# Kernel tuning notes

Hardware: AMD Instinct MI355X
Metric: run time of the kernel (lower is better)

Reference implementation:

```python
import jax, jax.numpy as jnp
import numpy as np

N, P, Q, H_DIM, HEADS, D = 4096, 128, 128, 256, 8, 64  # D = graph_dim // heads


def setup_inputs() -> dict:
    key = jax.random.key(0)
    ks = jax.random.split(key, 6)
    s = 0.05  # small scale to keep tanh/softmax in a sane range
    return {
        "x_prices": jax.random.normal(ks[0], (N, P), jnp.float32),
        "x_news": jax.random.normal(ks[1], (N, Q), jnp.float32),
        "W_bil": jax.random.normal(ks[2], (H_DIM, P, Q), jnp.float32) * s,
        "b_bil": jax.random.normal(ks[3], (H_DIM,), jnp.float32) * s,
        "Wt": jax.random.normal(ks[4], (HEADS, D, H_DIM), jnp.float32) * s,
        "a_vec": jax.random.normal(ks[5], (HEADS, 2 * D), jnp.float32) * s,
    }


def reference(x_prices, x_news, W_bil, b_bil, Wt, a_vec):
    # nn.Bilinear: out[n,h] = sum_pq x_prices[n,p] W[h,p,q] x_news[n,q] + b[h]
    x = jnp.einsum('np,hpq,nq->nh', x_prices, W_bil, x_news) + b_bil  # (N, hidden)

    # Per-head linear transform: fc_transform (no bias). Wt: (heads, d, hidden)
    xt = jnp.einsum('nh,kdh->knd', x, Wt)  # (heads, N, d)

    # Attention score a . [x_i, x_j] split into src/dst halves -> broadcast add
    d = Wt.shape[1]
    a_src, a_dst = a_vec[:, :d], a_vec[:, d:]
    s_src = jnp.einsum('knd,kd->kn', xt, a_src)  # (heads, N)
    s_dst = jnp.einsum('knd,kd->kn', xt, a_dst)  # (heads, N)
    scores = s_src[:, :, None] + s_dst[:, None, :]  # (heads, N, N)
    scores = jnp.where(scores >= 0, scores, 0.2 * scores)  # LeakyReLU(0.2)

    attn = jax.nn.softmax(scores, axis=-1)  # softmax over neighbors j
    out = jnp.einsum('knm,kmd->knd', attn, xt)  # (heads, N, d)

    # Concatenate head outputs on feature dim, then tanh
    out = jnp.transpose(out, (1, 0, 2)).reshape(xt.shape[1], -1)  # (N, heads*d)
    return jnp.tanh(out)
```

## Files before the change

kernel.cpp:

```cpp
#include <hip/hip_runtime.h>
#include <hip/hip_bf16.h>

typedef unsigned short ushort;
typedef unsigned int uint;
typedef unsigned long long u64;
typedef _Float16 f16;

#define NN 4096
#define PP 128
#define QQ 128
#define HD 256
#define KH 8
#define DD 64
#define KK 16384

typedef _Float16 f16x2 __attribute__((ext_vector_type(2)));
typedef _Float16 f16x4 __attribute__((ext_vector_type(4)));
typedef _Float16 f16x8 __attribute__((ext_vector_type(8)));
typedef __fp16 fp16x2 __attribute__((ext_vector_type(2)));
typedef float f32x4 __attribute__((ext_vector_type(4)));

__device__ inline void async_lds16(const void* g, void* l) {
  __builtin_amdgcn_global_load_lds(
      (const __attribute__((address_space(1))) unsigned int*)g,
      (__attribute__((address_space(3))) unsigned int*)l, 16, 0, 0);
}

__global__ __launch_bounds__(256) void k0_split2(
    const float* __restrict__ W, const float* __restrict__ Wt,
    f16* __restrict__ hiW, f16* __restrict__ loW,
    f16* __restrict__ hiT, f16* __restrict__ loT) {
  const int i = (blockIdx.x * 256 + threadIdx.x) * 4;
  const float* src;
  f16 *hi, *lo;
  int off;
  if (i < HD * PP * QQ) { src = W; hi = hiW; lo = loW; off = i; }
  else { src = Wt; hi = hiT; lo = loT; off = i - HD * PP * QQ; }
  const float4 w = *(const float4*)&src[off];
  const float wf[4] = {w.x, w.y, w.z, w.w};
  f16x4 hv, lv;
#pragma unroll
  for (int j = 0; j < 4; ++j) {
    const f16 h = (f16)wf[j];
    hv[j] = h;
    lv[j] = (f16)(wf[j] - (float)h);
  }
  *(f16x4*)&hi[off] = hv;
  *(f16x4*)&lo[off] = lv;
}

__global__ __launch_bounds__(256) void k_zero4(float* __restrict__ p) {
  const int i = (blockIdx.x * 256 + threadIdx.x) * 4;
  *(float4*)&p[i] = make_float4(0.f, 0.f, 0.f, 0.f);
}

__global__ __launch_bounds__(256, 2) void k1_bilinear(
    const float* __restrict__ xp, const float* __restrict__ xn,
    const f16* __restrict__ Whi, const f16* __restrict__ Wlo,
    float* __restrict__ xout) {
  __shared__ f16 whi[256 * 32];
  __shared__ f16 wlo[256 * 32];
  __shared__ f16 zhi[128 * 40];
  __shared__ float xpt[8][128];

  const int t = threadIdx.x;
  const int n0 = blockIdx.x * 128;
  const int kb = blockIdx.y * (KK / 16);
  const int pb = kb >> 7;

  for (int idx = t; idx < 1024; idx += 256) {
    const int p = idx & 7, n = idx >> 3;
    xpt[p][n] = xp[(size_t)(n0 + n) * PP + pb + p];
  }

  const int l = t & 63, w = t >> 6;
  const int wr = (w >> 1) * 64, wc = (w & 1) * 128;

  int aoff[4], boff[8];
#pragma unroll
  for (int i = 0; i < 4; ++i)
    aoff[i] = (wr + i * 16 + (l & 15)) * 40 + (l >> 4) * 8;
#pragma unroll
  for (int j = 0; j < 8; ++j) {
    const int hr = wc + j * 16 + (l & 15);
    boff[j] = hr * 32 + (((l >> 4) ^ ((hr ^ (hr >> 2)) & 3)) * 8);
  }

  const int shb = t >> 2, seg = t & 3;
  int gsw[4];
#pragma unroll
  for (int g = 0; g < 4; ++g) {
    const int r = shb + 64 * g;
    gsw[g] = seg ^ ((r ^ (r >> 2)) & 3);
  }

  const int zn = t >> 1, zko = (t & 1) * 16;

  f32x4 acc[4][8];
#pragma unroll
  for (int i = 0; i < 4; ++i)
#pragma unroll
    for (int j = 0; j < 8; ++j) acc[i][j] = (f32x4)0.f;

  for (int c = 0; c < 32; ++c) {
    const int kc = kb + c * 32;
    const int pl = c >> 2;
    const int q0 = (c & 3) * 32;

    __syncthreads();

#pragma unroll
    for (int g = 0; g < 4; ++g) {
      const int r = shb + 64 * g;
      async_lds16(Whi + (size_t)r * KK + kc + gsw[g] * 8, whi + r * 32 + seg * 8);
      async_lds16(Wlo + (size_t)r * KK + kc + gsw[g] * 8, wlo + r * 32 + seg * 8);
    }

    {
      const float xpv = xpt[pl][zn];
      const float* xr = xn + (size_t)(n0 + zn) * QQ + q0 + zko;
      float4 v0 = ((const float4*)xr)[0];
      float4 v1 = ((const float4*)xr)[1];
      float4 v2 = ((const float4*)xr)[2];
      float4 v3 = ((const float4*)xr)[3];
      float zz[16] = {v0.x, v0.y, v0.z, v0.w, v1.x, v1.y, v1.z, v1.w,
                      v2.x, v2.y, v2.z, v2.w, v3.x, v3.y, v3.z, v3.w};
      union { uint u[8]; uint4 q[2]; } ph;
#pragma unroll
      for (int j = 0; j < 8; ++j) {
        union { fp16x2 h; uint u; } cv;
        cv.h = __builtin_amdgcn_cvt_pkrtz(xpv * zz[2 * j], xpv * zz[2 * j + 1]);
        ph.u[j] = cv.u;
      }
      const int zo = zn * 40 + zko;
      *(uint4*)&zhi[zo] = ph.q[0];
      *(uint4*)&zhi[zo + 8] = ph.q[1];
    }

    __syncthreads();

    f16x8 Ah[4];
#pragma unroll
    for (int i = 0; i < 4; ++i) Ah[i] = *(const f16x8*)&zhi[aoff[i]];
#pragma unroll
    for (int j = 0; j < 8; ++j) {
      const f16x8 Bh = *(const f16x8*)&whi[boff[j]];
      const f16x8 Bl = *(const f16x8*)&wlo[boff[j]];
#pragma unroll
      for (int i = 0; i < 4; ++i)
        acc[i][j] = __builtin_amdgcn_mfma_f32_16x16x32_f16(Ah[i], Bh, acc[i][j], 0, 0, 0);
#pragma unroll
      for (int i = 0; i < 4; ++i)
        acc[i][j] = __builtin_amdgcn_mfma_f32_16x16x32_f16(Ah[i], Bl, acc[i][j], 0, 0, 0);
    }
  }

#pragma unroll
  for (int i = 0; i < 4; ++i)
#pragma unroll
    for (int j = 0; j < 8; ++j) {
      const int row = n0 + wr + i * 16 + (l >> 4) * 4;
      const int col = wc + j * 16 + (l & 15);
#pragma unroll
      for (int r = 0; r < 4; ++r)
        atomicAdd(&xout[(size_t)(row + r) * HD + col], acc[i][j][r]);
    }
}

__global__ __launch_bounds__(256) void k23_xt(
    const float* __restrict__ x, const float* __restrict__ bb,
    const f16* __restrict__ Wthi, const f16* __restrict__ Wtlo,
    float* __restrict__ xt) {
  __shared__ f16 ah[64 * 40];
  __shared__ f16 bh[128 * 32];
  __shared__ f16 bl[128 * 32];
  const int t = threadIdx.x;
  const int n0 = blockIdx.x * 64;
  const int c0 = blockIdx.y * 128;
  const int l = t & 63, w = t >> 6;
  const int wn = (w & 1) * 32, wcc = (w >> 1) * 64;

  int aoff[2], boff[4];
#pragma unroll
  for (int i = 0; i < 2; ++i)
    aoff[i] = (wn + i * 16 + (l & 15)) * 40 + (l >> 4) * 8;
#pragma unroll
  for (int j = 0; j < 4; ++j) {
    const int hr = wcc + j * 16 + (l & 15);
    boff[j] = hr * 32 + (((l >> 4) ^ ((hr ^ (hr >> 2)) & 3)) * 8);
  }

  f32x4 acc[2][4];
#pragma unroll
  for (int i = 0; i < 2; ++i)
#pragma unroll
    for (int j = 0; j < 4; ++j) acc[i][j] = (f32x4)0.f;

  for (int kc = 0; kc < HD; kc += 32) {
    __syncthreads();
    {
      const int row = t >> 2, sg = t & 3;
      const float* xr = &x[(size_t)(n0 + row) * HD + kc + sg * 8];
      const float4 xa = ((const float4*)xr)[0];
      const float4 xb = ((const float4*)xr)[1];
      const float4 ba = *(const float4*)&bb[kc + sg * 8];
      const float4 bv = *(const float4*)&bb[kc + sg * 8 + 4];
      f16x8 o;
      o[0] = (f16)(xa.x + ba.x); o[1] = (f16)(xa.y + ba.y);
      o[2] = (f16)(xa.z + ba.z); o[3] = (f16)(xa.w + ba.w);
      o[4] = (f16)(xb.x + bv.x); o[5] = (f16)(xb.y + bv.y);
      o[6] = (f16)(xb.z + bv.z); o[7] = (f16)(xb.w + bv.w);
      *(f16x8*)&ah[row * 40 + sg * 8] = o;
    }
#pragma unroll
    for (int g = 0; g < 2; ++g) {
      const int slot = g * 256 + t;
      const int col = slot >> 2, ps = slot & 3;
      const int ls = ps ^ ((col ^ (col >> 2)) & 3);
      *(uint4*)&bh[col * 32 + ps * 8] =
          *(const uint4*)&Wthi[(size_t)(c0 + col) * HD + kc + ls * 8];
      *(uint4*)&bl[col * 32 + ps * 8] =
          *(const uint4*)&Wtlo[(size_t)(c0 + col) * HD + kc + ls * 8];
    }
    __syncthreads();
    f16x8 Af[2];
#pragma unroll
    for (int i = 0; i < 2; ++i) Af[i] = *(const f16x8*)&ah[aoff[i]];
#pragma unroll
    for (int j = 0; j < 4; ++j) {
      const f16x8 Bh = *(const f16x8*)&bh[boff[j]];
      const f16x8 Bl = *(const f16x8*)&bl[boff[j]];
#pragma unroll
      for (int i = 0; i < 2; ++i)
        acc[i][j] = __builtin_amdgcn_mfma_f32_16x16x32_f16(Af[i], Bh, acc[i][j], 0, 0, 0);
#pragma unroll
      for (int i = 0; i < 2; ++i)
        acc[i][j] = __builtin_amdgcn_mfma_f32_16x16x32_f16(Af[i], Bl, acc[i][j], 0, 0, 0);
    }
  }
#pragma unroll
  for (int i = 0; i < 2; ++i)
#pragma unroll
    for (int j = 0; j < 4; ++j) {
      const int row = n0 + wn + i * 16 + (l >> 4) * 4;
      const int colg = c0 + wcc + j * 16 + (l & 15);
      const int k = colg >> 6, d = colg & 63;
#pragma unroll
      for (int r = 0; r < 4; ++r)
        xt[((size_t)(k * NN + row + r)) * DD + d] = acc[i][j][r];
    }
}

__global__ __launch_bounds__(256) void k3_scores(
    const float* __restrict__ xt, const float* __restrict__ av,
    float* __restrict__ ssrc, float* __restrict__ sdst) {
  const int tid = blockIdx.x * 256 + threadIdx.x;
  const int k = tid >> 12;
  const float* xr = xt + (long)tid * DD;
  const float* a = av + k * (2 * DD);
  float s1 = 0.f, s2 = 0.f;
#pragma unroll
  for (int d = 0; d < DD; d += 4) {
    const float4 xv = *(const float4*)&xr[d];
    const float4 a1 = *(const float4*)&a[d];
    const float4 a2 = *(const float4*)&a[DD + d];
    s1 += xv.x * a1.x + xv.y * a1.y + xv.z * a1.z + xv.w * a1.w;
    s2 += xv.x * a2.x + xv.y * a2.y + xv.z * a2.z + xv.w * a2.w;
  }
  ssrc[tid] = s1;
  sdst[tid] = s2;
}

__global__ __launch_bounds__(256) void k4_rank(
    const float* __restrict__ sdst, float* __restrict__ vsorted,
    int* __restrict__ perm) {
  __shared__ u64 kv[4096];
  const int k = blockIdx.y, t = threadIdx.x;
  for (int i = t; i < 4096; i += 256) {
    const uint u = __float_as_uint(sdst[k * NN + i]);
    const uint key = (u & 0x80000000u) ? ~u : (u | 0x80000000u);
    kv[i] = ((u64)key << 32) | (uint)i;
  }
  __syncthreads();
  const int m = blockIdx.x * 256 + t;
  const u64 my = kv[m];
  int cnt = 0;
#pragma unroll 16
  for (int j = 0; j < 4096; ++j) cnt += (kv[j] < my) ? 1 : 0;
  const uint key = (uint)(my >> 32);
  const uint u = (key & 0x80000000u) ? (key ^ 0x80000000u) : ~key;
  vsorted[k * NN + cnt] = __uint_as_float(u);
  perm[k * NN + cnt] = (int)(my & 0xFFFFFFFFu);
}

__global__ __launch_bounds__(64) void k4b_chunksum(
    const float* __restrict__ vs, const int* __restrict__ perm,
    const float* __restrict__ xt, float* __restrict__ Chi, float* __restrict__ Clo) {
  __shared__ float rows[64][64];
  __shared__ float eh[64], el[64];
  const int c = blockIdx.x, k = blockIdx.y, t = threadIdx.x;
  const int base = k * NN + c * 64;
  {
    const float v = vs[base + t];
    eh[t] = __expf(v);
    el[t] = __expf(0.2f * v);
  }
#pragma unroll
  for (int r = 0; r < 16; ++r) {
    const int i = r * 4 + (t >> 4);
    const int p = perm[base + i];
    *(float4*)&rows[i][(t & 15) * 4] =
        *(const float4*)&xt[((size_t)(k * NN + p)) * DD + (t & 15) * 4];
  }
  __syncthreads();
  float shi = 0.f, slo = 0.f, whs = 0.f, wls = 0.f;
#pragma unroll 8
  for (int i = 0; i < 64; ++i) {
    const float val = rows[i][t];
    shi += eh[i] * val; slo += el[i] * val;
    whs += eh[i]; wls += el[i];
  }
  const int cb = (k * 64 + c) * 65;
  Chi[cb + t] = shi;
  Clo[cb + t] = slo;
  if (t == 0) { Chi[cb + 64] = whs; Clo[cb + 64] = wls; }
}

__global__ __launch_bounds__(128) void k4c_scan(
    const float* __restrict__ Chi, const float* __restrict__ Clo,
    float* __restrict__ ChiS, float* __restrict__ CloS) {
  __shared__ float schi[64 * 65];
  __shared__ float sclo[64 * 65];
  const int k = blockIdx.x, t = threadIdx.x;
  for (int idx = t; idx < 4160; idx += 128) {
    schi[idx] = Chi[k * 4160 + idx];
    sclo[idx] = Clo[k * 4160 + idx];
  }
  __syncthreads();
  if (t >= 65) return;
  float run = 0.f;
  for (int c = 0; c < 64; ++c) {
    CloS[(k * 64 + c) * 65 + t] = run;
    run += sclo[c * 65 + t];
  }
  run = 0.f;
  for (int c = 63; c >= 0; --c) {
    run += schi[c * 65 + t];
    ChiS[(k * 64 + c) * 65 + t] = run;
  }
}

__global__ __launch_bounds__(64) void k4d_expand(
    const float* __restrict__ vs, const int* __restrict__ perm,
    const float* __restrict__ xt, const float* __restrict__ ChiS,
    const float* __restrict__ CloS, float* __restrict__ Phi,
    float* __restrict__ Plo) {
  __shared__ float rows[64][64];
  __shared__ float eh[64], el[64];
  const int c = blockIdx.x, k = blockIdx.y, t = threadIdx.x;
  const int base = k * NN + c * 64;
  const int cb = (k * 64 + c) * 65;
  {
    const float v = vs[base + t];
    eh[t] = __expf(v);
    el[t] = __expf(0.2f * v);
  }
#pragma unroll
  for (int r = 0; r < 16; ++r) {
    const int i = r * 4 + (t >> 4);
    const int p = perm[base + i];
    *(float4*)&rows[i][(t & 15) * 4] =
        *(const float4*)&xt[((size_t)(k * NN + p)) * DD + (t & 15) * 4];
  }
  __syncthreads();
  float run = CloS[cb + t];
  float wrun = CloS[cb + 64];
  for (int i = 0; i < 64; ++i) {
    const size_t rb = ((size_t)(k * 4097) + c * 64 + i) * 65;
    Plo[rb + t] = run;
    if (t == 0) Plo[rb + 64] = wrun;
    run += el[i] * rows[i][t];
    wrun += el[i];
  }
  if (c == 63) {
    const size_t rb = ((size_t)(k * 4097) + 4096) * 65;
    Plo[rb + t] = run;
    if (t == 0) Plo[rb + 64] = wrun;
  }
  run = (c < 63) ? ChiS[cb + 65 + t] : 0.f;
  wrun = (c < 63) ? ChiS[cb + 65 + 64] : 0.f;
  for (int i = 63; i >= 0; --i) {
    run += eh[i] * rows[i][t];
    wrun += eh[i];
    const size_t rb = ((size_t)(k * 4097) + c * 64 + i) * 65;
    Phi[rb + t] = run;
    if (t == 0) Phi[rb + 64] = wrun;
  }
  if (c == 63) {
    const size_t rb = ((size_t)(k * 4097) + 4096) * 65;
    Phi[rb + t] = 0.f;
    if (t == 0) Phi[rb + 64] = 0.f;
  }
}

__global__ __launch_bounds__(256) void k6_final(
    const float* __restrict__ ssrc, const float* __restrict__ vsorted,
    const float* __restrict__ Phi, const float* __restrict__ Plo,
    float* __restrict__ out) {
  __shared__ float vsh[4096];
  __shared__ int posSh[4];
  const int t = threadIdx.x;
  const int q0 = blockIdx.x * 4;
  const int k = q0 >> 12;
  for (int idx = t; idx < 1024; idx += 256)
    *(float4*)&vsh[idx * 4] = *(const float4*)&vsorted[k * NN + idx * 4];
  __syncthreads();
  if (t < 4) {
    const float thr = -ssrc[q0 + t];
    int lo = 0, hi = 4096;
    while (lo < hi) {
      const int mid = (lo + hi) >> 1;
      if (vsh[mid] < thr) lo = mid + 1; else hi = mid;
    }
    posSh[t] = lo;
  }
  __syncthreads();
  const int qi = q0 + (t >> 6);
  const int d = t & 63;
  const int n = qi & 4095;
  const float u = ssrc[qi];
  const size_t rb = ((size_t)(k * 4097) + posSh[t >> 6]) * 65;
  const float eu = __expf(u), el = __expf(0.2f * u);
  const float num = eu * Phi[rb + d] + el * Plo[rb + d];
  const float den = eu * Phi[rb + 64] + el * Plo[rb + 64];
  out[(size_t)n * (KH * DD) + k * DD + d] = tanhf(num / den);
}

extern "C" void kernel_launch(void* const* d_in, const int* in_sizes, int n_in,
                              void* d_out, int out_size, void* d_ws, size_t ws_size,
                              hipStream_t stream) {
  const float* xp = (const float*)d_in[0];
  const float* xn = (const float*)d_in[1];
  const float* W = (const float*)d_in[2];
  const float* bb = (const float*)d_in[3];
  const float* Wt = (const float*)d_in[4];
  const float* av = (const float*)d_in[5];
  float* out = (float*)d_out;

  char* ws = (char*)d_ws;
  f16* Whi    = (f16*)(ws);
  f16* Wlo    = (f16*)(ws + 8388608);
  float* Phi  = (float*)(ws);
  float* Plo  = (float*)(ws + 8522240);
  float* x    = (float*)(ws + 17044480);
  float* xt   = (float*)(ws + 21238784);
  f16* Wthi   = (f16*)(ws + 31724544);
  f16* Wtlo   = (f16*)(ws + 31986688);
  float* ssrc = (float*)(ws + 32248832);
  float* sdst = (float*)(ws + 32379904);
  float* vsort= (float*)(ws + 32510976);
  int*   perm = (int*)  (ws + 32642048);
  float* Chi  = (float*)(ws + 32773120);
  float* Clo  = (float*)(ws + 32906240);
  float* ChiS = (float*)(ws + 33039360);
  float* CloS = (float*)(ws + 33172480);

  k0_split2<<<(HD * PP * QQ + KH * DD * HD) / 1024, 256, 0, stream>>>(
      W, Wt, Whi, Wlo, Wthi, Wtlo);
  k_zero4<<<(NN * HD) / 1024, 256, 0, stream>>>(x);
  k1_bilinear<<<dim3(NN / 128, 16), 256, 0, stream>>>(xp, xn, Whi, Wlo, x);
  k23_xt<<<dim3(NN / 64, 4), 256, 0, stream>>>(x, bb, Wthi, Wtlo, xt);
  k3_scores<<<(KH * NN) / 256, 256, 0, stream>>>(xt, av, ssrc, sdst);
  k4_rank<<<dim3(16, KH), 256, 0, stream>>>(sdst, vsort, perm);
  k4b_chunksum<<<dim3(64, KH), 64, 0, stream>>>(vsort, perm, xt, Chi, Clo);
  k4c_scan<<<KH, 128, 0, stream>>>(Chi, Clo, ChiS, CloS);
  k4d_expand<<<dim3(64, KH), 64, 0, stream>>>(vsort, perm, xt, ChiS, CloS, Phi, Plo);
  k6_final<<<(KH * NN) / 4, 256, 0, stream>>>(ssrc, vsort, Phi, Plo, out);
}
```

Baseline: 290.4 us.

## Fuse zeroing and score kernels, double bilinear block to 512 threads

Zeroing of the bilinear output is folded into the weight-split kernel, and the attention score dot products are computed from MFMA accumulators inside the xt kernel through a shared-memory reduction, removing two launches and a reread of xt. The bilinear kernel now uses 512 threads covering 256 rows per block, so each W tile loaded into LDS is reused across twice as many rows, halving W traffic and the number of atomic partial-sum blocks. The larger block raises LDS use and register pressure under launch_bounds(512,2), and the hidden bilinear body must index rows consistently with the new tiling.

```diff
diff --git a/kernel.cpp b/kernel.cpp
--- a/kernel.cpp
+++ b/kernel.cpp
@@ -29,8 +29,11 @@
 __global__ __launch_bounds__(256) void k0_split2(
     const float* __restrict__ W, const float* __restrict__ Wt,
     f16* __restrict__ hiW, f16* __restrict__ loW,
-    f16* __restrict__ hiT, f16* __restrict__ loT) {
-  const int i = (blockIdx.x * 256 + threadIdx.x) * 4;
+    f16* __restrict__ hiT, f16* __restrict__ loT, float* __restrict__ xz) {
+  const int tid = blockIdx.x * 256 + threadIdx.x;
+  const int i = tid * 4;
+  if (tid < (NN * HD) / 4)
+    *(float4*)&xz[i] = make_float4(0.f, 0.f, 0.f, 0.f);
   const float* src;
   f16 *hi, *lo;
   int off;
@@ -49,32 +52,28 @@
   *(f16x4*)&lo[off] = lv;
 }
 
-__global__ __launch_bounds__(256) void k_zero4(float* __restrict__ p) {
-  const int i = (blockIdx.x * 256 + threadIdx.x) * 4;
-  *(float4*)&p[i] = make_float4(0.f, 0.f, 0.f, 0.f);
-}
-
-__global__ __launch_bounds__(256, 2) void k1_bilinear(
+__global__ __launch_bounds__(512, 2) void k1_bilinear(
     const float* __restrict__ xp, const float* __restrict__ xn,
     const f16* __restrict__ Whi, const f16* __restrict__ Wlo,
     float* __restrict__ xout) {
   __shared__ f16 whi[256 * 32];
   __shared__ f16 wlo[256 * 32];
-  __shared__ f16 zhi[128 * 40];
-  __shared__ float xpt[8][128];
+  __shared__ f16 zhi[256 * 40];
+  __shared__ float xpt[8][256];
 
   const int t = threadIdx.x;
-  const int n0 = blockIdx.x * 128;
+  const int n0 = blockIdx.x * 256;
   const int kb = blockIdx.y * (KK / 16);
   const int pb = kb >> 7;
 
-  for (int idx = t; idx < 1024; idx += 256) {
+  for (int idx = t; idx < 2048; idx += 512) {
     const int p = idx & 7, n = idx >> 3;
     xpt[p][n] = xp[(size_t)(n0 + n) * PP + pb + p];
   }
 
   const int l = t & 63, w = t >> 6;
-  const int wr = (w >> 1) * 64, wc = (w & 1) * 128;
+  const int wr = (w >> 1) * 64;
+  const int wc = (w & 1) * 128;
 
   int aoff[4], boff[8];
 #pragma unroll
@@ -87,10 +86,10 @@
   }
 
   const int shb = t >> 2, seg = t & 3;
-  int gsw[4];
-#pragma unroll
-  for (int g = 0; g < 4; ++g) {
-    const int r = shb + 64 * g;
+  int gsw[2];
+#pragma unroll
+  for (int g = 0; g < 2; ++g) {
+    const int r = shb + 128 * g;
     gsw[g] = seg ^ ((r ^ (r >> 2)) & 3);
   }
 
@@ -110,8 +109,8 @@
     __syncthreads();
 
 #pragma unroll
-    for (int g = 0; g < 4; ++g) {
-      const int r = shb + 64 * g;
+    for (int g = 0; g < 2; ++g) {
+      const int r = shb + 128 * g;
       async_lds16(Whi + (size_t)r * KK + kc + gsw[g] * 8, whi + r * 32 + seg * 8);
       async_lds16(Wlo + (size_t)r * KK + kc + gsw[g] * 8, wlo + r * 32 + seg * 8);
     }
@@ -170,10 +169,13 @@
 __global__ __launch_bounds__(256) void k23_xt(
     const float* __restrict__ x, const float* __restrict__ bb,
     const f16* __restrict__ Wthi, const f16* __restrict__ Wtlo,
-    float* __restrict__ xt) {
+    const float* __restrict__ av, float* __restrict__ xt,
+    float* __restrict__ ssrc, float* __restrict__ sdst) {
   __shared__ f16 ah[64 * 40];
   __shared__ f16 bh[128 * 32];
   __shared__ f16 bl[128 * 32];
+  __shared__ float red1[2][64][17];
+  __shared__ float red2[2][64][17];
   const int t = threadIdx.x;
   const int n0 = blockIdx.x * 64;
   const int c0 = blockIdx.y * 128;
@@ -238,6 +240,32 @@
         acc[i][j] = __builtin_amdgcn_mfma_f32_16x16x32_f16(Af[i], Bl, acc[i][j], 0, 0, 0);
     }
   }
+
+  const int hh = w >> 1;
+  const int khead = (c0 >> 6) + hh;
+  float a1v[4], a2v[4];
+#pragma unroll
+  for (int j = 0; j < 4; ++j) {
+    const int d = j * 16 + (l & 15);
+    a1v[j] = av[khead * (2 * DD) + d];
+    a2v[j] = av[khead * (2 * DD) + DD + d];
+  }
+
+#pragma unroll
+  for (int i = 0; i < 2; ++i)
+#pragma unroll
+    for (int r = 0; r < 4; ++r) {
+      const int rowl = wn + i * 16 + (l >> 4) * 4 + r;
+      float p1 = 0.f, p2 = 0.f;
+#pragma unroll
+      for (int j = 0; j < 4; ++j) {
+        p1 += acc[i][j][r] * a1v[j];
+        p2 += acc[i][j][r] * a2v[j];
+      }
+      red1[hh][rowl][l & 15] = p1;
+      red2[hh][rowl][l & 15] = p2;
+    }
+
 #pragma unroll
   for (int i = 0; i < 2; ++i)
 #pragma unroll
@@ -249,26 +277,20 @@
       for (int r = 0; r < 4; ++r)
         xt[((size_t)(k * NN + row + r)) * DD + d] = acc[i][j][r];
     }
-}
-
-__global__ __launch_bounds__(256) void k3_scores(
-    const float* __restrict__ xt, const float* __restrict__ av,
-    float* __restrict__ ssrc, float* __restrict__ sdst) {
-  const int tid = blockIdx.x * 256 + threadIdx.x;
-  const int k = tid >> 12;
-  const float* xr = xt + (long)tid * DD;
-  const float* a = av + k * (2 * DD);
-  float s1 = 0.f, s2 = 0.f;
-#pragma unroll
-  for (int d = 0; d < DD; d += 4) {
-    const float4 xv = *(const float4*)&xr[d];
-    const float4 a1 = *(const float4*)&a[d];
-    const float4 a2 = *(const float4*)&a[DD + d];
-    s1 += xv.x * a1.x + xv.y * a1.y + xv.z * a1.z + xv.w * a1.w;
-    s2 += xv.x * a2.x + xv.y * a2.y + xv.z * a2.z + xv.w * a2.w;
-  }
-  ssrc[tid] = s1;
-  sdst[tid] = s2;
+
+  __syncthreads();
+  {
+    const int hh2 = t >> 7;
+    const int which = (t >> 6) & 1;
+    const int row = t & 63;
+    const float* rp = which ? &red2[hh2][row][0] : &red1[hh2][row][0];
+    float s = 0.f;
+#pragma unroll
+    for (int g = 0; g < 16; ++g) s += rp[g];
+    const int kk = (c0 >> 6) + hh2;
+    if (which) sdst[kk * NN + n0 + row] = s;
+    else ssrc[kk * NN + n0 + row] = s;
+  }
 }
 
 __global__ __launch_bounds__(256) void k4_rank(
@@ -466,11 +488,9 @@
   float* CloS = (float*)(ws + 33172480);
 
   k0_split2<<<(HD * PP * QQ + KH * DD * HD) / 1024, 256, 0, stream>>>(
-      W, Wt, Whi, Wlo, Wthi, Wtlo);
-  k_zero4<<<(NN * HD) / 1024, 256, 0, stream>>>(x);
-  k1_bilinear<<<dim3(NN / 128, 16), 256, 0, stream>>>(xp, xn, Whi, Wlo, x);
-  k23_xt<<<dim3(NN / 64, 4), 256, 0, stream>>>(x, bb, Wthi, Wtlo, xt);
-  k3_scores<<<(KH * NN) / 256, 256, 0, stream>>>(xt, av, ssrc, sdst);
+      W, Wt, Whi, Wlo, Wthi, Wtlo, x);
+  k1_bilinear<<<dim3(NN / 256, 16), 512, 0, stream>>>(xp, xn, Whi, Wlo, x);
+  k23_xt<<<dim3(NN / 64, 4), 256, 0, stream>>>(x, bb, Wthi, Wtlo, av, xt, ssrc, sdst);
   k4_rank<<<dim3(16, KH), 256, 0, stream>>>(sdst, vsort, perm);
   k4b_chunksum<<<dim3(64, KH), 64, 0, stream>>>(vsort, perm, xt, Chi, Clo);
   k4c_scan<<<KH, 128, 0, stream>>>(Chi, Clo, ChiS, CloS);
```

After: 301.6 us. +3.8%, slower.
